# Kernel optimization log

Hardware: AMD Instinct MI355X
Metric: run time of the kernel (lower is better)

The kernel has to match this reference:

```python
import jax, jax.numpy as jnp
import numpy as np

BN_EPS = 1e-5
NUM_ROUTING_ITERS = 3


def _bn(x, gamma, beta, axes):
    # training-mode batch norm (torch default train mode): batch statistics
    mean = x.mean(axes, keepdims=True)
    var = x.var(axes, keepdims=True)
    return (x - mean) * jax.lax.rsqrt(var + BN_EPS) * gamma + beta


def _squash(x):
    # squash over last dim: sn * x / ((1+sn) * sqrt(sn))
    sn = jnp.sum(x * x, axis=-1, keepdims=True)
    return sn * x / ((1.0 + sn) * jnp.sqrt(sn))


def setup_inputs() -> dict:
    key = jax.random.key(0)
    ks = jax.random.split(key, 16)
    B, N = 4, 2048          # batch, num_points
    P, Q = 1024, 16         # prim_caps_size, prim_vec_size
    L, V = 64, 64           # latent_caps_size, latent_vec_size
    OUT = 40
    s = 0.02
    return {
        "x": jax.random.normal(ks[0], (B, 3, N), dtype=jnp.float32),
        # ConvLayer
        "w1": jax.random.normal(ks[1], (64, 3), dtype=jnp.float32) * s,
        "b1": jnp.zeros((64,), jnp.float32),
        "g1": jnp.ones((64,), jnp.float32),
        "be1": jnp.zeros((64,), jnp.float32),
        "w2": jax.random.normal(ks[2], (128, 64), dtype=jnp.float32) * s,
        "b2": jnp.zeros((128,), jnp.float32),
        "g2": jnp.ones((128,), jnp.float32),
        "be2": jnp.zeros((128,), jnp.float32),
        # PrimaryPointCapsLayer: Q parallel conv1d(128->P, k=1)+BN branches, stacked
        "w3": jax.random.normal(ks[3], (Q, P, 128), dtype=jnp.float32) * s,
        "b3": jnp.zeros((Q, P), jnp.float32),
        "g3": jnp.ones((Q, P), jnp.float32),
        "be3": jnp.zeros((Q, P), jnp.float32),
        # LatentCapsLayer routing weights
        "Wr": jax.random.normal(ks[4], (L, P, V, Q), dtype=jnp.float32) * 0.01,
        # classifier head
        "fc_w": jax.random.normal(ks[5], (OUT, L * V), dtype=jnp.float32) * s,
        "fc_b": jnp.zeros((OUT,), jnp.float32),
    }


def reference(x, w1, b1, g1, be1, w2, b2, g2, be2, w3, b3, g3, be3, Wr, fc_w, fc_b):
    B = x.shape[0]
    # ConvLayer: two 1x1 conv1d + BN + ReLU
    h = jnp.einsum("oc,bcn->bon", w1, x) + b1[None, :, None]
    h = jax.nn.relu(_bn(h, g1[None, :, None], be1[None, :, None], (0, 2)))
    h = jnp.einsum("oc,bcn->bon", w2, h) + b2[None, :, None]
    h = jax.nn.relu(_bn(h, g2[None, :, None], be2[None, :, None], (0, 2)))  # [B,128,N]

    # PrimaryPointCapsLayer: Q branches of conv1d+BN+global maxpool, vectorized
    u = jnp.einsum("qpc,bcn->bqpn", w3, h) + b3[None, :, :, None]  # [B,Q,P,N]
    u = _bn(u, g3[None, :, :, None], be3[None, :, :, None], (0, 3))
    u = u.max(axis=-1)                      # global maxpool -> [B,Q,P]
    u = jnp.transpose(u, (0, 2, 1))         # stack dim=2 in torch -> [B,P,Q]
    u = _squash(u)                          # squash over prim_vec

    # LatentCapsLayer dynamic routing
    u_hat = jnp.einsum("lpvq,bpq->blpv", Wr, u)   # [B,L,P,V]
    u_hat_d = jax.lax.stop_gradient(u_hat)
    L, P = Wr.shape[0], Wr.shape[1]
    b_ij = jnp.zeros((B, L, P), u_hat.dtype)
    for _ in range(NUM_ROUTING_ITERS - 1):
        c_ij = jax.nn.softmax(b_ij, axis=1)
        v_j = _squash(jnp.einsum("blp,blpv->blv", c_ij, u_hat_d))
        b_ij = b_ij + jnp.einsum("blv,blpv->blp", v_j, u_hat_d)
    c_ij = jax.nn.softmax(b_ij, axis=1)
    v_j = _squash(jnp.einsum("blp,blpv->blv", c_ij, u_hat))  # [B,L,V]

    presence = jnp.linalg.norm(v_j, axis=2)                   # [B,L]
    logits = v_j.reshape(B, -1) @ fc_w.T + fc_b               # [B,OUT]
    return (logits, presence)
```

## Files before the change

kernel.cpp:

```cpp
#include <hip/hip_runtime.h>
#include <math.h>

#define BN_EPS 1e-5f

typedef __attribute__((ext_vector_type(8))) _Float16 half8;
typedef __attribute__((ext_vector_type(4))) float f32x4;
#define SPLIT_S  2048.0f
#define INV_S    (1.0f/2048.0f)

__global__ void k_conv1(const float* __restrict__ x, const float* __restrict__ w1,
                        float* __restrict__ y1) {
    int bn = blockIdx.x * 256 + threadIdx.x;
    int o  = blockIdx.y;
    int b = bn >> 11, n = bn & 2047;
    const float* xb = x + (size_t)b * 6144 + n;
    y1[o * 8192 + bn] = w1[o*3+0]*xb[0] + w1[o*3+1]*xb[2048] + w1[o*3+2]*xb[4096];
}

__global__ void k_stats(const float* __restrict__ y, float* __restrict__ mean,
                        float* __restrict__ inv) {
    int c = blockIdx.x, t = threadIdx.x;
    float s = 0.f, ss = 0.f;
    const float4* src = (const float4*)(y + c * 8192);
    for (int i = t; i < 2048; i += 256) {
        float4 v = src[i];
        s += v.x + v.y + v.z + v.w;
        ss = fmaf(v.x, v.x, fmaf(v.y, v.y, fmaf(v.z, v.z, fmaf(v.w, v.w, ss))));
    }
    __shared__ float rs[256], rss[256];
    rs[t] = s; rss[t] = ss;
    __syncthreads();
    for (int off = 128; off > 0; off >>= 1) {
        if (t < off) { rs[t] += rs[t+off]; rss[t] += rss[t+off]; }
        __syncthreads();
    }
    if (t == 0) {
        float m = rs[0] * (1.f/8192.f);
        float var = rss[0] * (1.f/8192.f) - m*m;
        mean[c] = m;
        inv[c]  = rsqrtf(var + BN_EPS);
    }
}

__global__ void k_bnrelu(const float* __restrict__ y, float* __restrict__ h,
                         const float* __restrict__ mean, const float* __restrict__ inv,
                         const float* __restrict__ g, const float* __restrict__ be, int total4) {
    int i = blockIdx.x * 256 + threadIdx.x;
    if (i >= total4) return;
    int c = i >> 11;
    float sc = inv[c] * g[c], sh = be[c] - mean[c] * sc;
    float4 v = *(const float4*)(y + i * 4);
    v.x = fmaxf(fmaf(v.x, sc, sh), 0.f);
    v.y = fmaxf(fmaf(v.y, sc, sh), 0.f);
    v.z = fmaxf(fmaf(v.z, sc, sh), 0.f);
    v.w = fmaxf(fmaf(v.w, sc, sh), 0.f);
    *(float4*)(h + i * 4) = v;
}

__global__ __launch_bounds__(256) void k_conv2(const float* __restrict__ h1,
                                               const float* __restrict__ w2,
                                               float* __restrict__ y2) {
    int bn0 = (blockIdx.x * 256 + threadIdx.x) * 4;
    int og0 = blockIdx.y * 8;
    float4 acc[8];
#pragma unroll
    for (int j = 0; j < 8; ++j) acc[j] = float4{0.f,0.f,0.f,0.f};
    for (int c = 0; c < 64; ++c) {
        float4 hv = *(const float4*)(h1 + c*8192 + bn0);
#pragma unroll
        for (int j = 0; j < 8; ++j) {
            float w = w2[(og0+j)*64 + c];
            acc[j].x = fmaf(w, hv.x, acc[j].x); acc[j].y = fmaf(w, hv.y, acc[j].y);
            acc[j].z = fmaf(w, hv.z, acc[j].z); acc[j].w = fmaf(w, hv.w, acc[j].w);
        }
    }
#pragma unroll
    for (int j = 0; j < 8; ++j) *(float4*)(y2 + (og0+j)*8192 + bn0) = acc[j];
}

__global__ void k_split_w3(const float* __restrict__ w, _Float16* __restrict__ hi,
                           _Float16* __restrict__ lo) {
    int i = (blockIdx.x * 256 + threadIdx.x) * 4;
    float4 d = *reinterpret_cast<const float4*>(w + i);
    float vs[4] = {d.x, d.y, d.z, d.w};
#pragma unroll
    for (int j = 0; j < 4; ++j) {
        _Float16 h = (_Float16)vs[j];
        hi[i + j] = h;
        lo[i + j] = (_Float16)((vs[j] - (float)h) * SPLIT_S);
    }
}

__global__ __launch_bounds__(256) void k_h2t_split(const float* __restrict__ y2,
        const float* __restrict__ mean, const float* __restrict__ inv,
        const float* __restrict__ g, const float* __restrict__ be,
        _Float16* __restrict__ hi, _Float16* __restrict__ lo) {
    __shared__ float tile[64][65];
    const int t = threadIdx.x;
    const int bn0 = blockIdx.x * 64, c0 = blockIdx.y * 64;
#pragma unroll
    for (int r = 0; r < 16; ++r) {
        int idx = r * 256 + t;
        int cl = idx >> 6, bnl = idx & 63;
        int c = c0 + cl;
        float v = y2[(size_t)c * 8192 + bn0 + bnl];
        v = (v - mean[c]) * inv[c] * g[c] + be[c];
        tile[cl][bnl] = v > 0.f ? v : 0.f;
    }
    __syncthreads();
#pragma unroll
    for (int r = 0; r < 16; ++r) {
        int idx = r * 256 + t;
        int bnl = idx >> 6, cl = idx & 63;
        float v = tile[cl][bnl];
        _Float16 h = (_Float16)v;
        size_t o = (size_t)(bn0 + bnl) * 128 + c0 + cl;
        hi[o] = h;
        lo[o] = (_Float16)((v - (float)h) * SPLIT_S);
    }
}

__global__ __launch_bounds__(256, 2) void k_caps(
        const _Float16* __restrict__ w3h, const _Float16* __restrict__ w3l,
        const _Float16* __restrict__ h2h, const _Float16* __restrict__ h2l,
        float* __restrict__ umax, float* __restrict__ umin,
        float* __restrict__ usum_b, float* __restrict__ usumsq_b) {
    const int lane = threadIdx.x & 63, wave = threadIdx.x >> 6;
    const int b = blockIdx.y;
    const int mrow = blockIdx.x * 64;
    const int r16 = lane & 15, kq = lane >> 4;

    half8 Ah[4][4], Al[4][4];
#pragma unroll
    for (int mt = 0; mt < 4; ++mt) {
        const size_t base = (size_t)(mrow + mt*16 + r16) * 128 + kq * 8;
#pragma unroll
        for (int ks = 0; ks < 4; ++ks) {
            Ah[mt][ks] = *reinterpret_cast<const half8*>(w3h + base + ks*32);
            Al[mt][ks] = *reinterpret_cast<const half8*>(w3l + base + ks*32);
        }
    }
    float mx[4][4], mn[4][4], sm[4][4], sq[4][4];
#pragma unroll
    for (int mt = 0; mt < 4; ++mt)
#pragma unroll
        for (int r = 0; r < 4; ++r) {
            mx[mt][r] = -3.4e38f; mn[mt][r] = 3.4e38f; sm[mt][r] = 0.f; sq[mt][r] = 0.f;
        }

    for (int j = 0; j < 32; ++j) {
        const int nt = j * 4 + wave;
        const size_t nb = (size_t)(b*2048 + nt*16 + r16) * 128 + kq * 8;
        f32x4 acc[4], accx[4];
#pragma unroll
        for (int mt = 0; mt < 4; ++mt) { acc[mt] = f32x4{0.f,0.f,0.f,0.f}; accx[mt] = f32x4{0.f,0.f,0.f,0.f}; }
#pragma unroll
        for (int ks = 0; ks < 4; ++ks) {
            half8 Bh = *reinterpret_cast<const half8*>(h2h + nb + ks*32);
            half8 Bl = *reinterpret_cast<const half8*>(h2l + nb + ks*32);
#pragma unroll
            for (int mt = 0; mt < 4; ++mt) {
                acc[mt]  = __builtin_amdgcn_mfma_f32_16x16x32_f16(Ah[mt][ks], Bh, acc[mt], 0, 0, 0);
                accx[mt] = __builtin_amdgcn_mfma_f32_16x16x32_f16(Ah[mt][ks], Bl, accx[mt], 0, 0, 0);
                accx[mt] = __builtin_amdgcn_mfma_f32_16x16x32_f16(Al[mt][ks], Bh, accx[mt], 0, 0, 0);
            }
        }
#pragma unroll
        for (int mt = 0; mt < 4; ++mt)
#pragma unroll
            for (int r = 0; r < 4; ++r) {
                float v = fmaf(accx[mt][r], INV_S, acc[mt][r]);
                mx[mt][r] = fmaxf(mx[mt][r], v);
                mn[mt][r] = fminf(mn[mt][r], v);
                sm[mt][r] += v;
                sq[mt][r] = fmaf(v, v, sq[mt][r]);
            }
    }
#pragma unroll
    for (int off = 8; off >= 1; off >>= 1)
#pragma unroll
        for (int mt = 0; mt < 4; ++mt)
#pragma unroll
            for (int r = 0; r < 4; ++r) {
                mx[mt][r] = fmaxf(mx[mt][r], __shfl_xor(mx[mt][r], off));
                mn[mt][r] = fminf(mn[mt][r], __shfl_xor(mn[mt][r], off));
                sm[mt][r] += __shfl_xor(sm[mt][r], off);
                sq[mt][r] += __shfl_xor(sq[mt][r], off);
            }
    __shared__ float sred[4][4][64];
    if (r16 == 0) {
#pragma unroll
        for (int mt = 0; mt < 4; ++mt)
#pragma unroll
            for (int r = 0; r < 4; ++r) {
                int row = mt*16 + kq*4 + r;
                sred[0][wave][row] = mx[mt][r];
                sred[1][wave][row] = mn[mt][r];
                sred[2][wave][row] = sm[mt][r];
                sred[3][wave][row] = sq[mt][r];
            }
    }
    __syncthreads();
    if (threadIdx.x < 64) {
        const int t = threadIdx.x;
        float M = sred[0][0][t], m = sred[1][0][t], s = sred[2][0][t], q = sred[3][0][t];
#pragma unroll
        for (int w = 1; w < 4; ++w) {
            M = fmaxf(M, sred[0][w][t]);
            m = fminf(m, sred[1][w][t]);
            s += sred[2][w][t];
            q += sred[3][w][t];
        }
        umax[b*16384 + mrow + t]     = M;
        umin[b*16384 + mrow + t]     = m;
        usum_b[b*16384 + mrow + t]   = s;
        usumsq_b[b*16384 + mrow + t] = q;
    }
}

__global__ void k_u(const float* __restrict__ umax, const float* __restrict__ umin,
                    const float* __restrict__ usum_b, const float* __restrict__ usumsq_b,
                    const float* __restrict__ g3, const float* __restrict__ be3,
                    float* __restrict__ u) {
    int tg = blockIdx.x * 256 + threadIdx.x;
    int b = tg >> 10, p = tg & 1023;
    float ub[16]; float sn = 0.f;
#pragma unroll
    for (int q = 0; q < 16; ++q) {
        int qp = q * 1024 + p;
        float s  = usum_b[qp] + usum_b[16384+qp] + usum_b[32768+qp] + usum_b[49152+qp];
        float ss = usumsq_b[qp] + usumsq_b[16384+qp] + usumsq_b[32768+qp] + usumsq_b[49152+qp];
        float mean  = s * (1.f/8192.f);
        float var   = ss * (1.f/8192.f) - mean*mean;
        float scale = g3[qp] * rsqrtf(var + BN_EPS);
        float val = (scale >= 0.f) ? umax[b*16384 + qp] : umin[b*16384 + qp];
        float vb = (val - mean) * scale + be3[qp];
        ub[q] = vb; sn = fmaf(vb, vb, sn);
    }
    float f = sqrtf(sn) / (1.f + sn);
#pragma unroll
    for (int q = 0; q < 16; ++q) u[tg*16 + q] = ub[q] * f;
}

__global__ __launch_bounds__(256) void k_uhat(const float* __restrict__ Wr,
                                              const float* __restrict__ u,
                                              float* __restrict__ uhat) {
    const int t = threadIdx.x;
    const int p0 = blockIdx.x * 4, l = blockIdx.y;
    __shared__ float wr[4][16][68];
    __shared__ float us[4][4][16];
    const float* src = Wr + ((size_t)l * 1024 + p0) * 1024;
#pragma unroll
    for (int it = 0; it < 4; ++it) {
        float4 d = *(const float4*)(src + (it*256 + t) * 4);
        int v = t >> 2, q0 = (t & 3) * 4;
        wr[it][q0  ][v] = d.x; wr[it][q0+1][v] = d.y;
        wr[it][q0+2][v] = d.z; wr[it][q0+3][v] = d.w;
    }
    {
        int p = t >> 6, bb = (t >> 4) & 3, q = t & 15;
        us[p][bb][q] = u[((size_t)bb * 1024 + p0 + p) * 16 + q];
    }
    __syncthreads();
    const int bb = t >> 6, v = t & 63;
#pragma unroll
    for (int p = 0; p < 4; ++p) {
        float acc = 0.f;
#pragma unroll
        for (int q = 0; q < 16; ++q) acc = fmaf(wr[p][q][v], us[p][bb][q], acc);
        uhat[((size_t)(bb * 64 + l) * 1024 + p0 + p) * 64 + v] = acc;
    }
}

__global__ void k_passA(const float* __restrict__ uhat, float* __restrict__ vout) {
    const int t = threadIdx.x;
    const int c4 = t & 15, pr = t >> 4;
    const float* base = uhat + (size_t)blockIdx.x * 65536;
    float4 acc = float4{0.f,0.f,0.f,0.f};
    for (int it = 0; it < 64; ++it) {
        float4 d = *(const float4*)(base + (pr + it*16) * 64 + c4 * 4);
        acc.x += d.x; acc.y += d.y; acc.z += d.z; acc.w += d.w;
    }
    __shared__ float red[16][68];
    *(float4*)&red[pr][c4 * 4] = acc;
    __syncthreads();
    if (t < 64) {
        float s = 0.f;
#pragma unroll
        for (int w = 0; w < 16; ++w) s += red[w][t];
        s *= (1.f/64.f);
        float sn = s * s;
#pragma unroll
        for (int off = 32; off >= 1; off >>= 1) sn += __shfl_xor(sn, off);
        vout[blockIdx.x * 64 + t] = s * sqrtf(sn) / (1.f + sn);
    }
}

__global__ __launch_bounds__(256) void k_route(const float* __restrict__ uhat,
                                               const float* __restrict__ vin,
                                               float* __restrict__ bij,
                                               float* __restrict__ part, const int read_b) {
    const int blk = blockIdx.x;
    const int b = blk >> 7, ch = blk & 127;
    const int p0 = ch * 8;
    const int t = threadIdx.x;
    const int v = t & 63, w = t >> 6;
    __shared__ float uh[64][68];
    __shared__ float vs[64][68];
    __shared__ float bl[64];
    __shared__ float cl[64];
    {
        const float* src = vin + b * 4096;
        for (int i = t; i < 1024; i += 256) {
            float4 d = *(const float4*)(src + i * 4);
            int l = i >> 4, v0 = (i & 15) * 4;
            vs[l][v0] = d.x; vs[l][v0+1] = d.y; vs[l][v0+2] = d.z; vs[l][v0+3] = d.w;
        }
    }
    float sacc[16];
#pragma unroll
    for (int j = 0; j < 16; ++j) sacc[j] = 0.f;

    for (int pp = 0; pp < 8; ++pp) {
        const int p = p0 + pp;
        __syncthreads();
        const float* src = uhat + (size_t)b * 4194304 + (size_t)p * 64;
        for (int i = t; i < 1024; i += 256) {
            int l = i >> 4, v0 = (i & 15) * 4;
            float4 d = *(const float4*)(src + (size_t)l * 65536 + v0);
            uh[l][v0] = d.x; uh[l][v0+1] = d.y; uh[l][v0+2] = d.z; uh[l][v0+3] = d.w;
        }
        __syncthreads();
#pragma unroll
        for (int i = 0; i < 16; ++i) {
            const int l = w * 16 + i;
            float prod = uh[l][v] * vs[l][v];
#pragma unroll
            for (int off = 32; off >= 1; off >>= 1) prod += __shfl_xor(prod, off);
            if (v == 0) {
                float bb = prod;
                if (read_b) bb += bij[(b * 64 + l) * 1024 + p];
                bl[l] = bb;
                if (!read_b) bij[(b * 64 + l) * 1024 + p] = bb;
            }
        }
        __syncthreads();
        if (w == 0) {
            float xv = bl[v];
            float m = xv;
#pragma unroll
            for (int off = 32; off >= 1; off >>= 1) m = fmaxf(m, __shfl_xor(m, off));
            float e = expf(xv - m);
            float sgm = e;
#pragma unroll
            for (int off = 32; off >= 1; off >>= 1) sgm += __shfl_xor(sgm, off);
            cl[v] = e / sgm;
        }
        __syncthreads();
#pragma unroll
        for (int j = 0; j < 16; ++j) {
            const int l = j * 4 + w;
            sacc[j] = fmaf(cl[l], uh[l][v], sacc[j]);
        }
    }
#pragma unroll
    for (int j = 0; j < 16; ++j) {
        const int l = j * 4 + w;
        part[((size_t)(b * 128 + ch) * 64 + l) * 64 + v] = sacc[j];
    }
}

__global__ void k_red_squash(const float* __restrict__ part, float* __restrict__ vout,
                             float* __restrict__ pres) {
    const int wv = blockIdx.x;
    const int b = wv >> 6, l = wv & 63;
    const int v = threadIdx.x;
    float acc = 0.f;
    for (int ch = 0; ch < 128; ++ch) acc += part[((size_t)(b * 128 + ch) * 64 + l) * 64 + v];
    float sn = acc * acc;
#pragma unroll
    for (int off = 32; off >= 1; off >>= 1) sn += __shfl_xor(sn, off);
    vout[wv * 64 + v] = acc * sqrtf(sn) / (1.f + sn);
    if (pres != nullptr && v == 0) pres[wv] = sn / (1.f + sn);
}

__global__ void k_logits(const float* __restrict__ vj, const float* __restrict__ fcw,
                         const float* __restrict__ fcb, float* __restrict__ out) {
    int wv = blockIdx.x * 4 + (threadIdx.x >> 6);
    int lane = threadIdx.x & 63;
    int b = wv / 40, o = wv % 40;
    const float* xv = vj + b * 4096;
    const float* wr = fcw + (size_t)o * 4096;
    float acc = 0.f;
    for (int i = lane; i < 4096; i += 64) acc = fmaf(xv[i], wr[i], acc);
#pragma unroll
    for (int off = 32; off >= 1; off >>= 1) acc += __shfl_xor(acc, off);
    if (lane == 0) out[b * 40 + o] = acc + fcb[o];
}

extern "C" void kernel_launch(void* const* d_in, const int* in_sizes, int n_in,
                              void* d_out, int out_size, void* d_ws, size_t ws_size,
                              hipStream_t stream) {
    const float* x   = (const float*)d_in[0];
    const float* w1  = (const float*)d_in[1];
    const float* g1  = (const float*)d_in[3];
    const float* be1 = (const float*)d_in[4];
    const float* w2  = (const float*)d_in[5];
    const float* g2  = (const float*)d_in[7];
    const float* be2 = (const float*)d_in[8];
    const float* w3  = (const float*)d_in[9];
    const float* g3  = (const float*)d_in[11];
    const float* be3 = (const float*)d_in[12];
    const float* Wr  = (const float*)d_in[13];
    const float* fcw = (const float*)d_in[14];
    const float* fcb = (const float*)d_in[15];
    float* out = (float*)d_out;

    float* ws       = (float*)d_ws;
    float* y1       = ws;
    float* y2       = y1 + 524288;
    float* mean1    = y2 + 1048576;
    float* inv1     = mean1 + 64;
    float* mean2    = inv1 + 64;
    float* inv2     = mean2 + 128;
    float* umax     = inv2 + 128;
    float* umin     = umax + 65536;
    float* usum_b   = umin + 65536;
    float* usumsq_b = usum_b + 65536;
    float* u        = usumsq_b + 65536;
    float* v1       = u + 65536;
    float* v2       = v1 + 16384;
    float* vj       = v2 + 16384;
    float* bij      = vj + 16384;
    float* part     = bij + 262144;
    float* uhat     = part + 2097152;
    _Float16* w3h = (_Float16*)uhat;
    _Float16* w3l = w3h + 2097152;
    _Float16* h2h = w3l + 2097152;
    _Float16* h2l = h2h + 1048576;

    k_conv1<<<dim3(32, 64), 256, 0, stream>>>(x, w1, y1);
    k_stats<<<64, 256, 0, stream>>>(y1, mean1, inv1);
    k_bnrelu<<<512, 256, 0, stream>>>(y1, y1, mean1, inv1, g1, be1, 131072);
    k_conv2<<<dim3(8, 16), 256, 0, stream>>>(y1, w2, y2);
    k_stats<<<128, 256, 0, stream>>>(y2, mean2, inv2);
    k_split_w3<<<2048, 256, 0, stream>>>(w3, w3h, w3l);
    k_h2t_split<<<dim3(128, 2), 256, 0, stream>>>(y2, mean2, inv2, g2, be2, h2h, h2l);
    k_caps<<<dim3(256, 4), 256, 0, stream>>>(w3h, w3l, h2h, h2l, umax, umin, usum_b, usumsq_b);
    k_u<<<16, 256, 0, stream>>>(umax, umin, usum_b, usumsq_b, g3, be3, u);
    k_uhat<<<dim3(256, 64), 256, 0, stream>>>(Wr, u, uhat);
    k_passA<<<256, 256, 0, stream>>>(uhat, v1);
    k_route<<<512, 256, 0, stream>>>(uhat, v1, bij, part, 0);
    k_red_squash<<<256, 64, 0, stream>>>(part, v2, nullptr);
    k_route<<<512, 256, 0, stream>>>(uhat, v2, bij, part, 1);
    k_red_squash<<<256, 64, 0, stream>>>(part, vj, out + 160);
    k_logits<<<40, 256, 0, stream>>>(vj, fcw, fcb, out);
}
```

Measured before the change: 767.8 us.

## Restructure caps GEMM with LDS double-buffered B tiles and retile several small kernels

```diff
diff --git a/kernel.cpp b/kernel.cpp
--- a/kernel.cpp
+++ b/kernel.cpp
@@ -10,11 +10,21 @@
 
 __global__ void k_conv1(const float* __restrict__ x, const float* __restrict__ w1,
                         float* __restrict__ y1) {
-    int bn = blockIdx.x * 256 + threadIdx.x;
-    int o  = blockIdx.y;
-    int b = bn >> 11, n = bn & 2047;
+    int i = blockIdx.x * 256 + threadIdx.x;
+    int o = i >> 11;
+    int bn4 = (i & 2047) * 4;
+    int b = bn4 >> 11, n = bn4 & 2047;
     const float* xb = x + (size_t)b * 6144 + n;
-    y1[o * 8192 + bn] = w1[o*3+0]*xb[0] + w1[o*3+1]*xb[2048] + w1[o*3+2]*xb[4096];
+    float4 x0 = *(const float4*)(xb);
+    float4 x1 = *(const float4*)(xb + 2048);
+    float4 x2 = *(const float4*)(xb + 4096);
+    float wa = w1[o*3+0], wb = w1[o*3+1], wc = w1[o*3+2];
+    float4 r;
+    r.x = wa*x0.x + wb*x1.x + wc*x2.x;
+    r.y = wa*x0.y + wb*x1.y + wc*x2.y;
+    r.z = wa*x0.z + wb*x1.z + wc*x2.z;
+    r.w = wa*x0.w + wb*x1.w + wc*x2.w;
+    *(float4*)(y1 + o * 8192 + bn4) = r;
 }
 
 __global__ void k_stats(const float* __restrict__ y, float* __restrict__ mean,
@@ -61,33 +71,37 @@
                                                const float* __restrict__ w2,
                                                float* __restrict__ y2) {
     int bn0 = (blockIdx.x * 256 + threadIdx.x) * 4;
-    int og0 = blockIdx.y * 8;
-    float4 acc[8];
-#pragma unroll
-    for (int j = 0; j < 8; ++j) acc[j] = float4{0.f,0.f,0.f,0.f};
+    int og0 = blockIdx.y * 4;
+    float4 acc[4];
+#pragma unroll
+    for (int j = 0; j < 4; ++j) acc[j] = float4{0.f,0.f,0.f,0.f};
     for (int c = 0; c < 64; ++c) {
         float4 hv = *(const float4*)(h1 + c*8192 + bn0);
 #pragma unroll
-        for (int j = 0; j < 8; ++j) {
+        for (int j = 0; j < 4; ++j) {
             float w = w2[(og0+j)*64 + c];
             acc[j].x = fmaf(w, hv.x, acc[j].x); acc[j].y = fmaf(w, hv.y, acc[j].y);
             acc[j].z = fmaf(w, hv.z, acc[j].z); acc[j].w = fmaf(w, hv.w, acc[j].w);
         }
     }
 #pragma unroll
-    for (int j = 0; j < 8; ++j) *(float4*)(y2 + (og0+j)*8192 + bn0) = acc[j];
+    for (int j = 0; j < 4; ++j) *(float4*)(y2 + (og0+j)*8192 + bn0) = acc[j];
 }
 
 __global__ void k_split_w3(const float* __restrict__ w, _Float16* __restrict__ hi,
                            _Float16* __restrict__ lo) {
-    int i = (blockIdx.x * 256 + threadIdx.x) * 4;
-    float4 d = *reinterpret_cast<const float4*>(w + i);
-    float vs[4] = {d.x, d.y, d.z, d.w};
-#pragma unroll
-    for (int j = 0; j < 4; ++j) {
-        _Float16 h = (_Float16)vs[j];
-        hi[i + j] = h;
-        lo[i + j] = (_Float16)((vs[j] - (float)h) * SPLIT_S);
+    int base = blockIdx.x * 256 + threadIdx.x;
+#pragma unroll
+    for (int it = 0; it < 4; ++it) {
+        int i = (base + it * 131072) * 4;
+        float4 d = *reinterpret_cast<const float4*>(w + i);
+        float vs[4] = {d.x, d.y, d.z, d.w};
+#pragma unroll
+        for (int j = 0; j < 4; ++j) {
+            _Float16 h = (_Float16)vs[j];
+            hi[i + j] = h;
+            lo[i + j] = (_Float16)((vs[j] - (float)h) * SPLIT_S);
+        }
     }
 }
 
@@ -127,12 +141,14 @@
         float* __restrict__ usum_b, float* __restrict__ usumsq_b) {
     const int lane = threadIdx.x & 63, wave = threadIdx.x >> 6;
     const int b = blockIdx.y;
-    const int mrow = blockIdx.x * 64;
+    const int mrow = blockIdx.x * 128 + wave * 32;
     const int r16 = lane & 15, kq = lane >> 4;
 
-    half8 Ah[4][4], Al[4][4];
-#pragma unroll
-    for (int mt = 0; mt < 4; ++mt) {
+    __shared__ _Float16 Bs[2][8][64][8];
+
+    half8 Ah[2][4], Al[2][4];
+#pragma unroll
+    for (int mt = 0; mt < 2; ++mt) {
         const size_t base = (size_t)(mrow + mt*16 + r16) * 128 + kq * 8;
 #pragma unroll
         for (int ks = 0; ks < 4; ++ks) {
@@ -140,33 +156,47 @@
             Al[mt][ks] = *reinterpret_cast<const half8*>(w3l + base + ks*32);
         }
     }
-    float mx[4][4], mn[4][4], sm[4][4], sq[4][4];
-#pragma unroll
-    for (int mt = 0; mt < 4; ++mt)
+    float mx[2][4], mn[2][4], sm[2][4], sq[2][4];
+#pragma unroll
+    for (int mt = 0; mt < 2; ++mt)
 #pragma unroll
         for (int r = 0; r < 4; ++r) {
             mx[mt][r] = -3.4e38f; mn[mt][r] = 3.4e38f; sm[mt][r] = 0.f; sq[mt][r] = 0.f;
         }
 
-    for (int j = 0; j < 32; ++j) {
-        const int nt = j * 4 + wave;
-        const size_t nb = (size_t)(b*2048 + nt*16 + r16) * 128 + kq * 8;
-        f32x4 acc[4], accx[4];
-#pragma unroll
-        for (int mt = 0; mt < 4; ++mt) { acc[mt] = f32x4{0.f,0.f,0.f,0.f}; accx[mt] = f32x4{0.f,0.f,0.f,0.f}; }
+    const int u0 = wave * 2;
+    const int ks0 = u0 >> 1;
+    const size_t srow = (size_t)(b*2048 + r16) * 128 + ks0 * 32 + kq * 8;
+
+    {
+        *reinterpret_cast<half8*>(&Bs[0][u0  ][lane][0]) = *reinterpret_cast<const half8*>(h2h + srow);
+        *reinterpret_cast<half8*>(&Bs[0][u0+1][lane][0]) = *reinterpret_cast<const half8*>(h2l + srow);
+    }
+    __syncthreads();
+
+    for (int nt = 0; nt < 128; ++nt) {
+        const int buf = nt & 1;
+        const int ntn = (nt + 1 < 128) ? nt + 1 : nt;
+        const size_t snext = srow + (size_t)ntn * 16 * 128;
+        half8 g0 = *reinterpret_cast<const half8*>(h2h + snext);
+        half8 g1 = *reinterpret_cast<const half8*>(h2l + snext);
+
+        f32x4 acc[2], accx[2];
+#pragma unroll
+        for (int mt = 0; mt < 2; ++mt) { acc[mt] = f32x4{0.f,0.f,0.f,0.f}; accx[mt] = f32x4{0.f,0.f,0.f,0.f}; }
 #pragma unroll
         for (int ks = 0; ks < 4; ++ks) {
-            half8 Bh = *reinterpret_cast<const half8*>(h2h + nb + ks*32);
-            half8 Bl = *reinterpret_cast<const half8*>(h2l + nb + ks*32);
-#pragma unroll
-            for (int mt = 0; mt < 4; ++mt) {
+            half8 Bh = *reinterpret_cast<const half8*>(&Bs[buf][ks*2  ][lane][0]);
+            half8 Bl = *reinterpret_cast<const half8*>(&Bs[buf][ks*2+1][lane][0]);
+#pragma unroll
+            for (int mt = 0; mt < 2; ++mt) {
                 acc[mt]  = __builtin_amdgcn_mfma_f32_16x16x32_f16(Ah[mt][ks], Bh, acc[mt], 0, 0, 0);
                 accx[mt] = __builtin_amdgcn_mfma_f32_16x16x32_f16(Ah[mt][ks], Bl, accx[mt], 0, 0, 0);
                 accx[mt] = __builtin_amdgcn_mfma_f32_16x16x32_f16(Al[mt][ks], Bh, accx[mt], 0, 0, 0);
             }
         }
 #pragma unroll
-        for (int mt = 0; mt < 4; ++mt)
+        for (int mt = 0; mt < 2; ++mt)
 #pragma unroll
             for (int r = 0; r < 4; ++r) {
                 float v = fmaf(accx[mt][r], INV_S, acc[mt][r]);
@@ -175,11 +205,15 @@
                 sm[mt][r] += v;
                 sq[mt][r] = fmaf(v, v, sq[mt][r]);
             }
-    }
+        *reinterpret_cast<half8*>(&Bs[buf^1][u0  ][lane][0]) = g0;
+        *reinterpret_cast<half8*>(&Bs[buf^1][u0+1][lane][0]) = g1;
+        __syncthreads();
+    }
+
 #pragma unroll
     for (int off = 8; off >= 1; off >>= 1)
 #pragma unroll
-        for (int mt = 0; mt < 4; ++mt)
+        for (int mt = 0; mt < 2; ++mt)
 #pragma unroll
             for (int r = 0; r < 4; ++r) {
                 mx[mt][r] = fmaxf(mx[mt][r], __shfl_xor(mx[mt][r], off));
@@ -187,34 +221,17 @@
                 sm[mt][r] += __shfl_xor(sm[mt][r], off);
                 sq[mt][r] += __shfl_xor(sq[mt][r], off);
             }
-    __shared__ float sred[4][4][64];
     if (r16 == 0) {
 #pragma unroll
-        for (int mt = 0; mt < 4; ++mt)
+        for (int mt = 0; mt < 2; ++mt)
 #pragma unroll
             for (int r = 0; r < 4; ++r) {
-                int row = mt*16 + kq*4 + r;
-                sred[0][wave][row] = mx[mt][r];
-                sred[1][wave][row] = mn[mt][r];
-                sred[2][wave][row] = sm[mt][r];
-                sred[3][wave][row] = sq[mt][r];
+                int qp = mrow + mt*16 + kq*4 + r;
+                umax[b*16384 + qp]     = mx[mt][r];
+                umin[b*16384 + qp]     = mn[mt][r];
+                usum_b[b*16384 + qp]   = sm[mt][r];
+                usumsq_b[b*16384 + qp] = sq[mt][r];
             }
-    }
-    __syncthreads();
-    if (threadIdx.x < 64) {
-        const int t = threadIdx.x;
-        float M = sred[0][0][t], m = sred[1][0][t], s = sred[2][0][t], q = sred[3][0][t];
-#pragma unroll
-        for (int w = 1; w < 4; ++w) {
-            M = fmaxf(M, sred[0][w][t]);
-            m = fminf(m, sred[1][w][t]);
-            s += sred[2][w][t];
-            q += sred[3][w][t];
-        }
-        umax[b*16384 + mrow + t]     = M;
-        umin[b*16384 + mrow + t]     = m;
-        usum_b[b*16384 + mrow + t]   = s;
-        usumsq_b[b*16384 + mrow + t] = q;
     }
 }
 
@@ -246,29 +263,33 @@
                                               const float* __restrict__ u,
                                               float* __restrict__ uhat) {
     const int t = threadIdx.x;
-    const int p0 = blockIdx.x * 4, l = blockIdx.y;
+    const int l = blockIdx.y;
     __shared__ float wr[4][16][68];
     __shared__ float us[4][4][16];
-    const float* src = Wr + ((size_t)l * 1024 + p0) * 1024;
-#pragma unroll
-    for (int it = 0; it < 4; ++it) {
-        float4 d = *(const float4*)(src + (it*256 + t) * 4);
-        int v = t >> 2, q0 = (t & 3) * 4;
-        wr[it][q0  ][v] = d.x; wr[it][q0+1][v] = d.y;
-        wr[it][q0+2][v] = d.z; wr[it][q0+3][v] = d.w;
-    }
-    {
-        int p = t >> 6, bb = (t >> 4) & 3, q = t & 15;
-        us[p][bb][q] = u[((size_t)bb * 1024 + p0 + p) * 16 + q];
-    }
-    __syncthreads();
     const int bb = t >> 6, v = t & 63;
-#pragma unroll
-    for (int p = 0; p < 4; ++p) {
-        float acc = 0.f;
-#pragma unroll
-        for (int q = 0; q < 16; ++q) acc = fmaf(wr[p][q][v], us[p][bb][q], acc);
-        uhat[((size_t)(bb * 64 + l) * 1024 + p0 + p) * 64 + v] = acc;
+    for (int sub = 0; sub < 8; ++sub) {
+        const int p0 = blockIdx.x * 32 + sub * 4;
+        const float* src = Wr + ((size_t)l * 1024 + p0) * 1024;
+        if (sub) __syncthreads();
+#pragma unroll
+        for (int it = 0; it < 4; ++it) {
+            float4 d = *(const float4*)(src + (it*256 + t) * 4);
+            int vv = t >> 2, q0 = (t & 3) * 4;
+            wr[it][q0  ][vv] = d.x; wr[it][q0+1][vv] = d.y;
+            wr[it][q0+2][vv] = d.z; wr[it][q0+3][vv] = d.w;
+        }
+        {
+            int p = t >> 6, b2 = (t >> 4) & 3, q = t & 15;
+            us[p][b2][q] = u[((size_t)b2 * 1024 + p0 + p) * 16 + q];
+        }
+        __syncthreads();
+#pragma unroll
+        for (int p = 0; p < 4; ++p) {
+            float acc = 0.f;
+#pragma unroll
+            for (int q = 0; q < 16; ++q) acc = fmaf(wr[p][q][v], us[p][bb][q], acc);
+            uhat[((size_t)(bb * 64 + l) * 1024 + p0 + p) * 64 + v] = acc;
+        }
     }
 }
 
@@ -439,16 +460,16 @@
     _Float16* h2h = w3l + 2097152;
     _Float16* h2l = h2h + 1048576;
 
-    k_conv1<<<dim3(32, 64), 256, 0, stream>>>(x, w1, y1);
+    k_conv1<<<512, 256, 0, stream>>>(x, w1, y1);
     k_stats<<<64, 256, 0, stream>>>(y1, mean1, inv1);
     k_bnrelu<<<512, 256, 0, stream>>>(y1, y1, mean1, inv1, g1, be1, 131072);
-    k_conv2<<<dim3(8, 16), 256, 0, stream>>>(y1, w2, y2);
+    k_conv2<<<dim3(8, 32), 256, 0, stream>>>(y1, w2, y2);
     k_stats<<<128, 256, 0, stream>>>(y2, mean2, inv2);
-    k_split_w3<<<2048, 256, 0, stream>>>(w3, w3h, w3l);
+    k_split_w3<<<512, 256, 0, stream>>>(w3, w3h, w3l);
     k_h2t_split<<<dim3(128, 2), 256, 0, stream>>>(y2, mean2, inv2, g2, be2, h2h, h2l);
-    k_caps<<<dim3(256, 4), 256, 0, stream>>>(w3h, w3l, h2h, h2l, umax, umin, usum_b, usumsq_b);
+    k_caps<<<dim3(128, 4), 256, 0, stream>>>(w3h, w3l, h2h, h2l, umax, umin, usum_b, usumsq_b);
     k_u<<<16, 256, 0, stream>>>(umax, umin, usum_b, usumsq_b, g3, be3, u);
-    k_uhat<<<dim3(256, 64), 256, 0, stream>>>(Wr, u, uhat);
+    k_uhat<<<dim3(32, 64), 256, 0, stream>>>(Wr, u, uhat);
     k_passA<<<256, 256, 0, stream>>>(uhat, v1);
     k_route<<<512, 256, 0, stream>>>(uhat, v1, bij, part, 0);
     k_red_squash<<<256, 64, 0, stream>>>(part, v2, nullptr);
```

Measured after the change: 709.1 us. 7.6% less time.
